# Optimization experiments

Measured on AMD Instinct MI355X. Metric: run time of the kernel, lower is better.

Reference implementation:

```python
import jax, jax.numpy as jnp
import numpy as np

NUM_HEADS = 16
EPS = 1e-5


def _ln(x, w, b):
    mu = jnp.mean(x, axis=-1, keepdims=True)
    var = jnp.mean((x - mu) ** 2, axis=-1, keepdims=True)
    return (x - mu) * jax.lax.rsqrt(var + EPS) * w + b


def _ada_ln(x, vol, lw, lb, gamma, beta, vs_w, vs_b):
    y = _ln(x, lw, lb)
    # volatility_scale: Linear(1,1) on vol[..., None] -> sigmoid
    vs = jax.nn.sigmoid(vol[..., None] * vs_w + vs_b)  # (B,S,1)
    return y * (1.0 + vs) * gamma + beta


def setup_inputs() -> dict:
    key = jax.random.key(0)
    ks = jax.random.split(key, 20)
    B, S, H = 8, 1024, 1024
    Hf = 4 * H
    Hg = H // 2
    w = lambda k, i, o: jax.random.normal(k, (i, o), jnp.float32) * 0.02
    inp = {
        'x': jax.random.normal(ks[0], (B, S, H), jnp.float32),
        'volatility': jax.random.uniform(ks[1], (B, S), jnp.float32),
        'Wq': w(ks[2], H, H), 'bq': jnp.zeros((H,), jnp.float32),
        'Wk': w(ks[3], H, H), 'bk': jnp.zeros((H,), jnp.float32),
        'Wv': w(ks[4], H, H), 'bv': jnp.zeros((H,), jnp.float32),
        'Wo': w(ks[5], H, H), 'bo': jnp.zeros((H,), jnp.float32),
        'ln1_w': jnp.ones((H,), jnp.float32), 'ln1_b': jnp.zeros((H,), jnp.float32),
        'gamma1': jnp.ones((), jnp.float32), 'beta1': jnp.zeros((), jnp.float32),
        'vs1_w': jnp.float32(0.3), 'vs1_b': jnp.float32(0.0),
        'ffn_w1': w(ks[6], H, Hf), 'ffn_b1': jnp.zeros((Hf,), jnp.float32),
        'ffn_w2': w(ks[7], Hf, H), 'ffn_b2': jnp.zeros((H,), jnp.float32),
        'gate_w1': w(ks[8], H, Hg), 'gate_b1': jnp.zeros((Hg,), jnp.float32),
        'gate_w2': w(ks[9], Hg, H), 'gate_b2': jnp.zeros((H,), jnp.float32),
        'ln2_w': jnp.ones((H,), jnp.float32), 'ln2_b': jnp.zeros((H,), jnp.float32),
        'gamma2': jnp.ones((), jnp.float32), 'beta2': jnp.zeros((), jnp.float32),
        'vs2_w': jnp.float32(0.3), 'vs2_b': jnp.float32(0.0),
    }
    return inp


def reference(x, volatility, Wq, bq, Wk, bk, Wv, bv, Wo, bo,
              ln1_w, ln1_b, gamma1, beta1, vs1_w, vs1_b,
              ffn_w1, ffn_b1, ffn_w2, ffn_b2,
              gate_w1, gate_b1, gate_w2, gate_b2,
              ln2_w, ln2_b, gamma2, beta2, vs2_w, vs2_b):
    B, S, H = x.shape
    nh = NUM_HEADS
    hd = H // nh
    scale = np.sqrt(hd).astype(np.float32)

    # self-attention (eval mode -> dropout is identity)
    Q = (x @ Wq + bq).reshape(B, S, nh, hd)
    K = (x @ Wk + bk).reshape(B, S, nh, hd)
    V = (x @ Wv + bv).reshape(B, S, nh, hd)
    scores = jnp.einsum('bqhd,bkhd->bhqk', Q, K) / scale
    attn = jax.nn.softmax(scores, axis=-1)
    ctx = jnp.einsum('bhqk,bkhd->bqhd', attn, V).reshape(B, S, H)
    attn_out = ctx @ Wo + bo

    x = x + attn_out
    x = _ada_ln(x, volatility, ln1_w, ln1_b, gamma1, beta1, vs1_w, vs1_b)

    # volatility-adaptive FFN (volatility present -> gated path)
    h = jax.nn.gelu(x @ ffn_w1 + ffn_b1, approximate=False)
    ffn_out = h @ ffn_w2 + ffn_b2
    g = jax.nn.sigmoid(jax.nn.relu(x @ gate_w1 + gate_b1) @ gate_w2 + gate_b2)
    ffn_res = ffn_out * g + x * (1.0 - g)

    x = x + ffn_res
    x = _ada_ln(x, volatility, ln2_w, ln2_b, gamma2, beta2, vs2_w, vs2_b)
    return x
```

## Files before the change

### kernel.cpp

```cpp
#include <hip/hip_runtime.h>
#include <hip/hip_bf16.h>
#include <math.h>


#define HDIM 1024
#define NHEAD 16
#define DHEAD 64
#define NBATCH 8
#define NSEQ 1024
#define NTOK (NBATCH * NSEQ)
#define QKVSTR 3072
#define LNEPS 1e-5f
#define LOG2E_8 0.180336880f

using f32x4 = __attribute__((ext_vector_type(4))) float;
using s16x8 = __attribute__((ext_vector_type(8))) short;
using u16x8 = __attribute__((ext_vector_type(8))) unsigned short;

enum { ACT_NONE = 0, ACT_GELU = 1, ACT_RELU = 2, ACT_SIG = 3 };

__device__ inline float bf2f(unsigned short u) {
    union { unsigned u; float f; } t; t.u = ((unsigned)u) << 16; return t.f;
}
__device__ inline unsigned short f2bf(float f) {
    __hip_bfloat16 h = __float2bfloat16(f);
    return *reinterpret_cast<unsigned short*>(&h);
}
__device__ inline float gelu_f(float t) {
    const float u = t * (0.7978845608f + 0.0356774081f * t * t);
    const float e = __expf(2.f * u);
    const float th = 1.f - 2.f / (e + 1.f);
    return 0.5f * t * (1.f + th);
}

#define GLDS16(g, l) __builtin_amdgcn_global_load_lds( \
    (__attribute__((address_space(1))) void*)(g),      \
    (__attribute__((address_space(3))) void*)(l), 16, 0, 0)
#define MFMA16(a, b, c) __builtin_amdgcn_mfma_f32_16x16x32_bf16(a, b, c, 0, 0, 0)
#define BAR() __builtin_amdgcn_s_barrier()
#define LGKM0() do { asm volatile("s_waitcnt lgkmcnt(0)" ::: "memory"); \
                     __builtin_amdgcn_sched_barrier(0); } while (0)

template<int N> __device__ __forceinline__ void vmwait() {
    asm volatile("s_waitcnt vmcnt(%0)" :: "i"(N) : "memory");
}

__global__ __launch_bounds__(256)
void cast_bf16_k(const float* __restrict__ in, unsigned short* __restrict__ out, int n4)
{
    for (int i = blockIdx.x * 256 + threadIdx.x; i < n4; i += gridDim.x * 256) {
        float4 v = ((const float4*)in)[i];
        ushort4 o;
        o.x = f2bf(v.x); o.y = f2bf(v.y); o.z = f2bf(v.z); o.w = f2bf(v.w);
        ((ushort4*)out)[i] = o;
    }
}

__global__ __launch_bounds__(256)
void concat3_k(const float* __restrict__ a, const float* __restrict__ b,
               const float* __restrict__ c, float* __restrict__ o)
{
    int i = blockIdx.x * 256 + threadIdx.x;
    o[i] = i < 1024 ? a[i] : (i < 2048 ? b[i - 1024] : c[i - 2048]);
}

__global__ __launch_bounds__(256)
void transpose_cast_k(const float* __restrict__ W, unsigned short* __restrict__ Wt,
                      int K, int N)
{
    __shared__ float tile[32][33];
    const int tx = threadIdx.x, ty = threadIdx.y;
    const int k0 = blockIdx.y * 32, n0 = blockIdx.x * 32;
#pragma unroll
    for (int r = 0; r < 32; r += 8)
        tile[ty + r][tx] = W[(size_t)(k0 + ty + r) * N + n0 + tx];
    __syncthreads();
#pragma unroll
    for (int r = 0; r < 32; r += 8)
        Wt[(size_t)(n0 + ty + r) * K + k0 + tx] = f2bf(tile[tx][ty + r]);
}

__global__ __launch_bounds__(256)
void transpose_cast4_k(const float* __restrict__ W0, const float* __restrict__ W1,
                       const float* __restrict__ W2, const float* __restrict__ W3,
                       unsigned short* __restrict__ Wt)
{
    __shared__ float tile[32][33];
    const int z = blockIdx.z;
    const float* W = z == 0 ? W0 : z == 1 ? W1 : z == 2 ? W2 : W3;
    unsigned short* dst = Wt + (size_t)z * HDIM * HDIM;
    const int tx = threadIdx.x, ty = threadIdx.y;
    const int k0 = blockIdx.y * 32, n0 = blockIdx.x * 32;
#pragma unroll
    for (int r = 0; r < 32; r += 8)
        tile[ty + r][tx] = W[(size_t)(k0 + ty + r) * HDIM + n0 + tx];
    __syncthreads();
#pragma unroll
    for (int r = 0; r < 32; r += 8)
        dst[(size_t)(n0 + ty + r) * HDIM + k0 + tx] = f2bf(tile[tx][ty + r]);
}

__global__ __launch_bounds__(256)
void transpose_v_k(const unsigned short* __restrict__ vb, unsigned short* __restrict__ vtb)
{
    __shared__ unsigned short t[64][72];
    const int tid = threadIdx.x;
    const int b = blockIdx.z, h = blockIdx.y;
    const int s0 = blockIdx.x * 64;
    {
        const int r = tid >> 3, c = (tid & 7) * 8;
        *(u16x8*)&t[r][c] =
            *(const u16x8*)&vb[((size_t)(b * NSEQ + s0 + r)) * QKVSTR + h * DHEAD + c];
        *(u16x8*)&t[r + 32][c] =
            *(const u16x8*)&vb[((size_t)(b * NSEQ + s0 + r + 32)) * QKVSTR + h * DHEAD + c];
    }
    __syncthreads();
    {
        const int d = tid & 63, sc = (tid >> 6) * 16;
        u16x8 o0, o1;
#pragma unroll
        for (int i = 0; i < 8; ++i) o0[i] = t[sc + i][d];
#pragma unroll
        for (int i = 0; i < 8; ++i) o1[i] = t[sc + 8 + i][d];
        unsigned short* dst = &vtb[((size_t)((b * NHEAD + h) * DHEAD + d)) * NSEQ + s0 + sc];
        *(u16x8*)dst = o0;
        *(u16x8*)(dst + 8) = o1;
    }
}

template<int BM, int ACT, bool HAS_ADD, bool OUT_BF>
__global__ __launch_bounds__(256, 4)
void gemm_hi_k(const unsigned short* __restrict__ A, const unsigned short* __restrict__ Bt,
               const float* __restrict__ bias, const float* __restrict__ add,
               void* __restrict__ Cv, int M, int N, int K, int nbx)
{
    constexpr int NREP = (BM == 128) ? 4 : 2;
    constexpr int AR = BM / 64;
    constexpr int VM = AR + 2;
    __shared__ alignas(16) unsigned short As[2][BM * 32];
    __shared__ alignas(16) unsigned short Bs[2][128 * 32];

    const int tid = threadIdx.x;
    const int lane = tid & 63;
    const int w = tid >> 6;
    const int wr = (BM == 128) ? (w >> 1) : 0;
    const int wcb = (BM == 128) ? ((w & 1) * 64) : (w * 32);
    const int chunk = gridDim.x >> 3;
    const int wg = (blockIdx.x & 7) * chunk + (blockIdx.x >> 3);
    const int m0 = (wg / nbx) * BM;
    const int n0 = (wg % nbx) * 128;

    const int fr = lane & 15;
    const int fo = lane >> 4;
    const int fo_swz8 = (fo ^ ((fr >> 1) & 3)) * 8;

    const int srow = tid >> 2;
    const int sg8 = ((tid & 3) ^ ((tid >> 3) & 3)) * 8;

    f32x4 acc[4][NREP] = {};

    auto stage = [&](int t) {
        const int buf = t & 1;
        const unsigned short* as_ = A + (size_t)(m0 + srow) * K + t * 32 + sg8;
        const unsigned short* bs_ = Bt + (size_t)(n0 + srow) * K + t * 32 + sg8;
        GLDS16(as_, &As[buf][(w * 16) * 32]);
        if constexpr (BM == 128)
            GLDS16(as_ + (size_t)64 * K, &As[buf][(64 + w * 16) * 32]);
        GLDS16(bs_, &Bs[buf][(w * 16) * 32]);
        GLDS16(bs_ + (size_t)64 * K, &Bs[buf][(64 + w * 16) * 32]);
    };

    const int NT = K / 32;
    stage(0);

    for (int t = 0; t < NT; ++t) {
        if (t + 1 < NT) { stage(t + 1); vmwait<VM>(); }
        else            { vmwait<0>(); }
        BAR();

        const int buf = t & 1;
        s16x8 af[4], bf[NREP];
#pragma unroll
        for (int i = 0; i < 4; ++i)
            af[i] = *(const s16x8*)(&As[buf][(wr * 64 + i * 16 + fr) * 32 + fo_swz8]);
#pragma unroll
        for (int j = 0; j < NREP; ++j)
            bf[j] = *(const s16x8*)(&Bs[buf][(wcb + j * 16 + fr) * 32 + fo_swz8]);

        __builtin_amdgcn_s_setprio(1);
#pragma unroll
        for (int i = 0; i < 4; ++i)
#pragma unroll
            for (int j = 0; j < NREP; ++j)
                acc[i][j] = MFMA16(af[i], bf[j], acc[i][j]);
        __builtin_amdgcn_s_setprio(0);

        LGKM0();
        BAR();
    }

    float bv[NREP];
#pragma unroll
    for (int j = 0; j < NREP; ++j)
        bv[j] = bias[n0 + wcb + j * 16 + fr];
#pragma unroll
    for (int i = 0; i < 4; ++i) {
#pragma unroll
        for (int j = 0; j < NREP; ++j) {
            const int gn = n0 + wcb + j * 16 + fr;
#pragma unroll
            for (int r = 0; r < 4; ++r) {
                const int gm = m0 + wr * 64 + i * 16 + fo * 4 + r;
                float t = acc[i][j][r] + bv[j];
                if (HAS_ADD) t += add[(size_t)gm * N + gn];
                if (ACT == ACT_GELU)      t = gelu_f(t);
                else if (ACT == ACT_RELU) t = fmaxf(t, 0.f);
                else if (ACT == ACT_SIG)  t = 1.f / (1.f + __expf(-t));
                if (OUT_BF) ((unsigned short*)Cv)[(size_t)gm * N + gn] = f2bf(t);
                else        ((float*)Cv)[(size_t)gm * N + gn] = t;
            }
        }
    }
}

__global__ __launch_bounds__(512, 6)
void attn_k(const unsigned short* __restrict__ QKVb, const unsigned short* __restrict__ Vtb,
            unsigned short* __restrict__ Cb)
{
    __shared__ alignas(16) unsigned short Ks[2][64 * 64];
    __shared__ alignas(16) unsigned short Vs[2][64 * 64];
    __shared__ alignas(16) unsigned short Ps[8][16 * 72];

    const int tid = threadIdx.x;
    const int lane = tid & 63;
    const int wid = tid >> 6;
    const int L = blockIdx.x;
    const int xcd = L & 7, s = L >> 3;
    const int bh = xcd + ((s >> 3) << 3);
    const int qt = s & 7;
    const int b = bh >> 4, h = bh & 15;
    const int q0 = qt * 128 + wid * 16;

    const int kcol = lane & 15;
    const int kofs = (lane >> 4) * 8;
    const size_t qoff = ((size_t)(b * NSEQ + q0 + kcol)) * QKVSTR + h * DHEAD + kofs;
    const s16x8 qf0 = *(const s16x8*)(QKVb + qoff);
    const s16x8 qf1 = *(const s16x8*)(QKVb + qoff + 32);

    f32x4 accO[4] = {};
    float mrow[4] = {-1e30f, -1e30f, -1e30f, -1e30f};
    float lsum[4] = {0.f, 0.f, 0.f, 0.f};

    const int lr = lane >> 3;
    const int swz8 = (((lane & 7) ^ lr)) * 8;
    const size_t kbase  = ((size_t)(b * NSEQ)) * QKVSTR + HDIM + h * DHEAD;
    const size_t vtbase = ((size_t)(bh * DHEAD)) * NSEQ;

    unsigned short* const pw = &Ps[wid][0];
    const int prow = (lane >> 4) * 4;

    auto stage = [&](int kt, int buf) {
        const int rowb = wid * 8;
        GLDS16(QKVb + kbase + (size_t)(kt * 64 + rowb + lr) * QKVSTR + swz8,
               Ks[buf] + rowb * 64);
        GLDS16(Vtb + vtbase + (size_t)(rowb + lr) * NSEQ + kt * 64 + swz8,
               Vs[buf] + rowb * 64);
    };

    stage(0, 0);
    asm volatile("s_waitcnt vmcnt(0)" ::: "memory");
    __syncthreads();

    for (int kt = 0; kt < NSEQ / 64; ++kt) {
        const int cur = kt & 1;
        if (kt + 1 < NSEQ / 64) stage(kt + 1, cur ^ 1);

        f32x4 sa[4];
#pragma unroll
        for (int jt = 0; jt < 4; ++jt) {
            const int kr = jt * 16 + kcol;
            const unsigned swz = ((unsigned)(kr & 7)) << 4;
            const s16x8 kf0 = *(const s16x8*)((const char*)Ks[cur] + kr * 128 + ((kofs * 2) ^ swz));
            const s16x8 kf1 = *(const s16x8*)((const char*)Ks[cur] + kr * 128 + ((64 + kofs * 2) ^ swz));
            f32x4 t = {};
            t = MFMA16(qf0, kf0, t);
            t = MFMA16(qf1, kf1, t);
            sa[jt] = t * LOG2E_8;
        }

        float lmax[4];
#pragma unroll
        for (int r = 0; r < 4; ++r)
            lmax[r] = fmaxf(fmaxf(sa[0][r], sa[1][r]), fmaxf(sa[2][r], sa[3][r]));
        const float guard = fmaxf(fmaxf(lmax[0] - mrow[0], lmax[1] - mrow[1]),
                                  fmaxf(lmax[2] - mrow[2], lmax[3] - mrow[3]));
        if (!__all(guard <= 8.f)) {
#pragma unroll
            for (int r = 0; r < 4; ++r) {
                float m = lmax[r];
                m = fmaxf(m, __shfl_xor(m, 1));
                m = fmaxf(m, __shfl_xor(m, 2));
                m = fmaxf(m, __shfl_xor(m, 4));
                m = fmaxf(m, __shfl_xor(m, 8));
                const float mn = fmaxf(mrow[r], m);
                const float corr = exp2f(mrow[r] - mn);
                mrow[r] = mn;
                lsum[r] *= corr;
#pragma unroll
                for (int dt = 0; dt < 4; ++dt) accO[dt][r] *= corr;
            }
        }
#pragma unroll
        for (int r = 0; r < 4; ++r) {
#pragma unroll
            for (int jt = 0; jt < 4; ++jt) {
                const float p = exp2f(sa[jt][r] - mrow[r]);
                pw[(prow + r) * 72 + jt * 16 + kcol] = f2bf(p);
                lsum[r] += p;
            }
        }

#pragma unroll
        for (int kc = 0; kc < 2; ++kc) {
            const s16x8 pa = *(const s16x8*)(pw + kcol * 72 + kc * 32 + kofs);
#pragma unroll
            for (int dt = 0; dt < 4; ++dt) {
                const int dr = dt * 16 + kcol;
                const unsigned swz = ((unsigned)(dr & 7)) << 4;
                const s16x8 vf = *(const s16x8*)((const char*)Vs[cur] + dr * 128 +
                                                 ((kc * 64 + kofs * 2) ^ swz));
                accO[dt] = MFMA16(pa, vf, accO[dt]);
            }
        }

        if (kt + 1 < NSEQ / 64) asm volatile("s_waitcnt vmcnt(0)" ::: "memory");
        __builtin_amdgcn_s_barrier();
    }

#pragma unroll
    for (int r = 0; r < 4; ++r) {
        lsum[r] += __shfl_xor(lsum[r], 1);
        lsum[r] += __shfl_xor(lsum[r], 2);
        lsum[r] += __shfl_xor(lsum[r], 4);
        lsum[r] += __shfl_xor(lsum[r], 8);
    }

    const size_t obase = ((size_t)(b * NSEQ + q0 + prow)) * HDIM + h * DHEAD;
#pragma unroll
    for (int r = 0; r < 4; ++r) {
        const float rl = 1.f / lsum[r];
#pragma unroll
        for (int dt = 0; dt < 4; ++dt)
            Cb[obase + (size_t)r * HDIM + dt * 16 + kcol] = f2bf(accO[dt][r] * rl);
    }
}

template<int MODE, bool WRITE_BF>
__global__ __launch_bounds__(256)
void adaln_k(const float* __restrict__ a,
             const unsigned short* __restrict__ fo_bf,
             const unsigned short* __restrict__ g_bf,
             const float* __restrict__ vol,
             const float* __restrict__ lw, const float* __restrict__ lb,
             const float* __restrict__ gm, const float* __restrict__ bt,
             const float* __restrict__ vsw, const float* __restrict__ vsb,
             float* __restrict__ out, unsigned short* __restrict__ out_bf)
{
    const int tok = blockIdx.x;
    const int tid = threadIdx.x;
    const size_t base = (size_t)tok * HDIM + tid * 4;
    float v[4];
    {
        float4 va = *(const float4*)&a[base];
        if (MODE == 1) {
            ushort4 uf = *(const ushort4*)&fo_bf[base];
            ushort4 ug = *(const ushort4*)&g_bf[base];
            float f0 = bf2f(uf.x), f1 = bf2f(uf.y), f2 = bf2f(uf.z), f3 = bf2f(uf.w);
            float g0 = bf2f(ug.x), g1 = bf2f(ug.y), g2 = bf2f(ug.z), g3 = bf2f(ug.w);
            v[0] = va.x * (2.f - g0) + f0 * g0;
            v[1] = va.y * (2.f - g1) + f1 * g1;
            v[2] = va.z * (2.f - g2) + f2 * g2;
            v[3] = va.w * (2.f - g3) + f3 * g3;
        } else {
            v[0] = va.x; v[1] = va.y; v[2] = va.z; v[3] = va.w;
        }
    }
    float sum = v[0] + v[1] + v[2] + v[3];
    float sq  = v[0]*v[0] + v[1]*v[1] + v[2]*v[2] + v[3]*v[3];
#pragma unroll
    for (int off = 32; off > 0; off >>= 1) {
        sum += __shfl_down(sum, off);
        sq  += __shfl_down(sq, off);
    }
    __shared__ float ssum[4], ssq[4];
    const int wid = tid >> 6, lane = tid & 63;
    if (lane == 0) { ssum[wid] = sum; ssq[wid] = sq; }
    __syncthreads();
    const float tsum = ssum[0] + ssum[1] + ssum[2] + ssum[3];
    const float tsq  = ssq[0]  + ssq[1]  + ssq[2]  + ssq[3];
    const float mu   = tsum * (1.f / 1024.f);
    const float var  = tsq * (1.f / 1024.f) - mu * mu;
    const float rstd = rsqrtf(var + LNEPS);
    const float vsv  = 1.f / (1.f + __expf(-(vol[tok] * vsw[0] + vsb[0])));
    const float sca  = (1.f + vsv) * gm[0];
    const float off2 = bt[0];
    const float4 lwv = *(const float4*)&lw[tid * 4];
    const float4 lbv = *(const float4*)&lb[tid * 4];
    float r0 = ((v[0] - mu) * rstd * lwv.x + lbv.x) * sca + off2;
    float r1 = ((v[1] - mu) * rstd * lwv.y + lbv.y) * sca + off2;
    float r2 = ((v[2] - mu) * rstd * lwv.z + lbv.z) * sca + off2;
    float r3 = ((v[3] - mu) * rstd * lwv.w + lbv.w) * sca + off2;
    *(float4*)&out[base] = make_float4(r0, r1, r2, r3);
    if (WRITE_BF) {
        ushort4 ob;
        ob.x = f2bf(r0); ob.y = f2bf(r1); ob.z = f2bf(r2); ob.w = f2bf(r3);
        *(ushort4*)&out_bf[base] = ob;
    }
}

extern "C" void kernel_launch(void* const* d_in, const int* in_sizes, int n_in,
                              void* d_out, int out_size, void* d_ws, size_t ws_size,
                              hipStream_t stream)
{
    (void)in_sizes; (void)n_in; (void)out_size; (void)ws_size;
    const float* x    = (const float*)d_in[0];
    const float* vol  = (const float*)d_in[1];
    const float* Wq   = (const float*)d_in[2];  const float* bq  = (const float*)d_in[3];
    const float* Wk   = (const float*)d_in[4];  const float* bk  = (const float*)d_in[5];
    const float* Wv   = (const float*)d_in[6];  const float* bv  = (const float*)d_in[7];
    const float* Wo   = (const float*)d_in[8];  const float* bo  = (const float*)d_in[9];
    const float* ln1w = (const float*)d_in[10]; const float* ln1b = (const float*)d_in[11];
    const float* gm1  = (const float*)d_in[12]; const float* be1 = (const float*)d_in[13];
    const float* vs1w = (const float*)d_in[14]; const float* vs1b = (const float*)d_in[15];
    const float* fw1  = (const float*)d_in[16]; const float* fb1 = (const float*)d_in[17];
    const float* fw2  = (const float*)d_in[18]; const float* fb2 = (const float*)d_in[19];
    const float* gw1  = (const float*)d_in[20]; const float* gb1 = (const float*)d_in[21];
    const float* gw2  = (const float*)d_in[22]; const float* gb2 = (const float*)d_in[23];
    const float* ln2w = (const float*)d_in[24]; const float* ln2b = (const float*)d_in[25];
    const float* gm2  = (const float*)d_in[26]; const float* be2 = (const float*)d_in[27];
    const float* vs2w = (const float*)d_in[28]; const float* vs2b = (const float*)d_in[29];

    char* w = (char*)d_ws;
    auto MB = [](size_t v) { return v << 20; };
    unsigned short* wtqkv = (unsigned short*)(w + MB(0));
    unsigned short* wto   = (unsigned short*)(w + MB(6));
    unsigned short* wtf1  = (unsigned short*)(w + MB(8));
    unsigned short* wtf2  = (unsigned short*)(w + MB(16));
    unsigned short* wtg1  = (unsigned short*)(w + MB(24));
    unsigned short* wtg2  = (unsigned short*)(w + MB(25));
    unsigned short* xb   = (unsigned short*)(w + MB(26));
    unsigned short* qkvb = (unsigned short*)(w + MB(42));
    unsigned short* vtb  = (unsigned short*)(w + MB(90));
    unsigned short* cxb  = (unsigned short*)(w + MB(106));
    float*          ao   = (float*)(w + MB(122));
    float*          x1   = (float*)(w + MB(42));
    unsigned short* x1b  = (unsigned short*)(w + MB(74));
    unsigned short* hb   = (unsigned short*)(w + MB(90));
    unsigned short* ffnb = (unsigned short*)(w + MB(154));
    unsigned short* ghb  = (unsigned short*)(w + MB(170));
    unsigned short* ggb  = (unsigned short*)(w + MB(26));
    float*          bqkv = (float*)(w + MB(184));

    dim3 blk(256);
    dim3 tb(32, 8);
    transpose_cast4_k<<<dim3(32, 32, 4), tb, 0, stream>>>(Wq, Wk, Wv, Wo, wtqkv);
    transpose_cast_k<<<dim3(4096/32, 1024/32), tb, 0, stream>>>(fw1, wtf1, 1024, 4096);
    transpose_cast_k<<<dim3(1024/32, 4096/32), tb, 0, stream>>>(fw2, wtf2, 4096, 1024);
    transpose_cast_k<<<dim3(512/32, 1024/32),  tb, 0, stream>>>(gw1, wtg1, 1024, 512);
    transpose_cast_k<<<dim3(1024/32, 512/32),  tb, 0, stream>>>(gw2, wtg2, 512, 1024);
    cast_bf16_k<<<2048, blk, 0, stream>>>(x, xb, NTOK * HDIM / 4);
    concat3_k<<<12, blk, 0, stream>>>(bq, bk, bv, bqkv);

    gemm_hi_k<128, ACT_NONE, false, true><<<dim3(24 * 64), blk, 0, stream>>>(
        xb, wtqkv, bqkv, nullptr, qkvb, NTOK, QKVSTR, HDIM, 24);
    transpose_v_k<<<dim3(NSEQ / 64, NHEAD, NBATCH), blk, 0, stream>>>(qkvb + 2048, vtb);
    attn_k<<<dim3(1024), 512, 0, stream>>>(qkvb, vtb, cxb);
    gemm_hi_k<64, ACT_NONE, true, false><<<dim3(128 * 8), blk, 0, stream>>>(
        cxb, wto, bo, x, ao, NTOK, HDIM, HDIM, 8);
    adaln_k<0, true><<<dim3(NTOK), blk, 0, stream>>>(
        ao, nullptr, nullptr, vol, ln1w, ln1b, gm1, be1, vs1w, vs1b, x1, x1b);
    gemm_hi_k<128, ACT_GELU, false, true><<<dim3(32 * 64), blk, 0, stream>>>(
        x1b, wtf1, fb1, nullptr, hb, NTOK, 4096, HDIM, 32);
    gemm_hi_k<64, ACT_NONE, false, true><<<dim3(128 * 8), blk, 0, stream>>>(
        hb, wtf2, fb2, nullptr, ffnb, NTOK, HDIM, 4096, 8);
    gemm_hi_k<64, ACT_RELU, false, true><<<dim3(128 * 4), blk, 0, stream>>>(
        x1b, wtg1, gb1, nullptr, ghb, NTOK, 512, HDIM, 4);
    gemm_hi_k<64, ACT_SIG, false, true><<<dim3(128 * 8), blk, 0, stream>>>(
        ghb, wtg2, gb2, nullptr, ggb, NTOK, HDIM, 512, 8);
    adaln_k<1, false><<<dim3(NTOK), blk, 0, stream>>>(
        x1, ffnb, ggb, vol, ln2w, ln2b, gm2, be2, vs2w, vs2b, (float*)d_out, nullptr);
}
```

Before: 463.9 us.

## Fuse FFN up-projection and gate first layer into one GEMM

Concatenates the transposed FFN W1 and gate W1 weights, and their biases, so that a single 128-row-tile GEMM produces both the GELU hidden and the ReLU gate hidden, using a per-column activation selector. A new lda parameter lets the downstream FFN2 and gate2 GEMMs read their halves from the shared 4608-wide buffer. This removes one kernel launch and a second pass over x1b, and replaces the small, poorly occupied gate GEMM with extra tiles in a large grid. It also drops the explicit LDS-count wait before the loop-end barrier and relies on compiler-inserted waits instead.

After: 473.0 us. About the same (+1.9%).

```diff
diff --git a/kernel.cpp b/kernel.cpp
--- a/kernel.cpp
+++ b/kernel.cpp
@@ -17,7 +17,7 @@
 using s16x8 = __attribute__((ext_vector_type(8))) short;
 using u16x8 = __attribute__((ext_vector_type(8))) unsigned short;
 
-enum { ACT_NONE = 0, ACT_GELU = 1, ACT_RELU = 2, ACT_SIG = 3 };
+enum { ACT_NONE = 0, ACT_GELU = 1, ACT_RELU = 2, ACT_SIG = 3, ACT_GR = 4 };
 
 __device__ inline float bf2f(unsigned short u) {
     union { unsigned u; float f; } t; t.u = ((unsigned)u) << 16; return t.f;
@@ -38,8 +38,6 @@
     (__attribute__((address_space(3))) void*)(l), 16, 0, 0)
 #define MFMA16(a, b, c) __builtin_amdgcn_mfma_f32_16x16x32_bf16(a, b, c, 0, 0, 0)
 #define BAR() __builtin_amdgcn_s_barrier()
-#define LGKM0() do { asm volatile("s_waitcnt lgkmcnt(0)" ::: "memory"); \
-                     __builtin_amdgcn_sched_barrier(0); } while (0)
 
 template<int N> __device__ __forceinline__ void vmwait() {
     asm volatile("s_waitcnt vmcnt(%0)" :: "i"(N) : "memory");
@@ -62,6 +60,14 @@
 {
     int i = blockIdx.x * 256 + threadIdx.x;
     o[i] = i < 1024 ? a[i] : (i < 2048 ? b[i - 1024] : c[i - 2048]);
+}
+
+__global__ __launch_bounds__(256)
+void concat2_k(const float* __restrict__ a, const float* __restrict__ b,
+               float* __restrict__ o)
+{
+    int i = blockIdx.x * 256 + threadIdx.x;
+    o[i] = i < 4096 ? a[i] : b[i - 4096];
 }
 
 __global__ __launch_bounds__(256)
@@ -132,7 +138,7 @@
 __global__ __launch_bounds__(256, 4)
 void gemm_hi_k(const unsigned short* __restrict__ A, const unsigned short* __restrict__ Bt,
                const float* __restrict__ bias, const float* __restrict__ add,
-               void* __restrict__ Cv, int M, int N, int K, int nbx)
+               void* __restrict__ Cv, int M, int N, int K, int lda, int nbx)
 {
     constexpr int NREP = (BM == 128) ? 4 : 2;
     constexpr int AR = BM / 64;
@@ -161,11 +167,11 @@
 
     auto stage = [&](int t) {
         const int buf = t & 1;
-        const unsigned short* as_ = A + (size_t)(m0 + srow) * K + t * 32 + sg8;
+        const unsigned short* as_ = A + (size_t)(m0 + srow) * lda + t * 32 + sg8;
         const unsigned short* bs_ = Bt + (size_t)(n0 + srow) * K + t * 32 + sg8;
         GLDS16(as_, &As[buf][(w * 16) * 32]);
         if constexpr (BM == 128)
-            GLDS16(as_ + (size_t)64 * K, &As[buf][(64 + w * 16) * 32]);
+            GLDS16(as_ + (size_t)64 * lda, &As[buf][(64 + w * 16) * 32]);
         GLDS16(bs_, &Bs[buf][(w * 16) * 32]);
         GLDS16(bs_ + (size_t)64 * K, &Bs[buf][(64 + w * 16) * 32]);
     };
@@ -195,7 +201,6 @@
                 acc[i][j] = MFMA16(af[i], bf[j], acc[i][j]);
         __builtin_amdgcn_s_setprio(0);
 
-        LGKM0();
         BAR();
     }
 
@@ -216,6 +221,7 @@
                 if (ACT == ACT_GELU)      t = gelu_f(t);
                 else if (ACT == ACT_RELU) t = fmaxf(t, 0.f);
                 else if (ACT == ACT_SIG)  t = 1.f / (1.f + __expf(-t));
+                else if (ACT == ACT_GR)   t = (gn < 4096) ? gelu_f(t) : fmaxf(t, 0.f);
                 if (OUT_BF) ((unsigned short*)Cv)[(size_t)gm * N + gn] = f2bf(t);
                 else        ((float*)Cv)[(size_t)gm * N + gn] = t;
             }
@@ -444,9 +450,9 @@
     auto MB = [](size_t v) { return v << 20; };
     unsigned short* wtqkv = (unsigned short*)(w + MB(0));
     unsigned short* wto   = (unsigned short*)(w + MB(6));
-    unsigned short* wtf1  = (unsigned short*)(w + MB(8));
-    unsigned short* wtf2  = (unsigned short*)(w + MB(16));
-    unsigned short* wtg1  = (unsigned short*)(w + MB(24));
+    unsigned short* wtfg  = (unsigned short*)(w + MB(8));
+    unsigned short* wtg1  = (unsigned short*)(w + MB(16));
+    unsigned short* wtf2  = (unsigned short*)(w + MB(17));
     unsigned short* wtg2  = (unsigned short*)(w + MB(25));
     unsigned short* xb   = (unsigned short*)(w + MB(26));
     unsigned short* qkvb = (unsigned short*)(w + MB(42));
@@ -455,38 +461,37 @@
     float*          ao   = (float*)(w + MB(122));
     float*          x1   = (float*)(w + MB(42));
     unsigned short* x1b  = (unsigned short*)(w + MB(74));
-    unsigned short* hb   = (unsigned short*)(w + MB(90));
-    unsigned short* ffnb = (unsigned short*)(w + MB(154));
-    unsigned short* ghb  = (unsigned short*)(w + MB(170));
+    unsigned short* hgb  = (unsigned short*)(w + MB(90));
+    unsigned short* ffnb = (unsigned short*)(w + MB(162));
     unsigned short* ggb  = (unsigned short*)(w + MB(26));
     float*          bqkv = (float*)(w + MB(184));
+    float*          bfg  = (float*)(w + MB(185));
 
     dim3 blk(256);
     dim3 tb(32, 8);
     transpose_cast4_k<<<dim3(32, 32, 4), tb, 0, stream>>>(Wq, Wk, Wv, Wo, wtqkv);
-    transpose_cast_k<<<dim3(4096/32, 1024/32), tb, 0, stream>>>(fw1, wtf1, 1024, 4096);
+    transpose_cast_k<<<dim3(4096/32, 1024/32), tb, 0, stream>>>(fw1, wtfg, 1024, 4096);
+    transpose_cast_k<<<dim3(512/32, 1024/32),  tb, 0, stream>>>(gw1, wtg1, 1024, 512);
     transpose_cast_k<<<dim3(1024/32, 4096/32), tb, 0, stream>>>(fw2, wtf2, 4096, 1024);
-    transpose_cast_k<<<dim3(512/32, 1024/32),  tb, 0, stream>>>(gw1, wtg1, 1024, 512);
     transpose_cast_k<<<dim3(1024/32, 512/32),  tb, 0, stream>>>(gw2, wtg2, 512, 1024);
     cast_bf16_k<<<2048, blk, 0, stream>>>(x, xb, NTOK * HDIM / 4);
     concat3_k<<<12, blk, 0, stream>>>(bq, bk, bv, bqkv);
+    concat2_k<<<18, blk, 0, stream>>>(fb1, gb1, bfg);
 
     gemm_hi_k<128, ACT_NONE, false, true><<<dim3(24 * 64), blk, 0, stream>>>(
-        xb, wtqkv, bqkv, nullptr, qkvb, NTOK, QKVSTR, HDIM, 24);
+        xb, wtqkv, bqkv, nullptr, qkvb, NTOK, QKVSTR, HDIM, HDIM, 24);
     transpose_v_k<<<dim3(NSEQ / 64, NHEAD, NBATCH), blk, 0, stream>>>(qkvb + 2048, vtb);
     attn_k<<<dim3(1024), 512, 0, stream>>>(qkvb, vtb, cxb);
     gemm_hi_k<64, ACT_NONE, true, false><<<dim3(128 * 8), blk, 0, stream>>>(
-        cxb, wto, bo, x, ao, NTOK, HDIM, HDIM, 8);
+        cxb, wto, bo, x, ao, NTOK, HDIM, HDIM, HDIM, 8);
     adaln_k<0, true><<<dim3(NTOK), blk, 0, stream>>>(
         ao, nullptr, nullptr, vol, ln1w, ln1b, gm1, be1, vs1w, vs1b, x1, x1b);
-    gemm_hi_k<128, ACT_GELU, false, true><<<dim3(32 * 64), blk, 0, stream>>>(
-        x1b, wtf1, fb1, nullptr, hb, NTOK, 4096, HDIM, 32);
+    gemm_hi_k<128, ACT_GR, false, true><<<dim3(36 * 64), blk, 0, stream>>>(
+        x1b, wtfg, bfg, nullptr, hgb, NTOK, 4608, HDIM, HDIM, 36);
     gemm_hi_k<64, ACT_NONE, false, true><<<dim3(128 * 8), blk, 0, stream>>>(
-        hb, wtf2, fb2, nullptr, ffnb, NTOK, HDIM, 4096, 8);
-    gemm_hi_k<64, ACT_RELU, false, true><<<dim3(128 * 4), blk, 0, stream>>>(
-        x1b, wtg1, gb1, nullptr, ghb, NTOK, 512, HDIM, 4);
+        hgb, wtf2, fb2, nullptr, ffnb, NTOK, HDIM, 4096, 4608, 8);
     gemm_hi_k<64, ACT_SIG, false, true><<<dim3(128 * 8), blk, 0, stream>>>(
-        ghb, wtg2, gb2, nullptr, ggb, NTOK, HDIM, 512, 8);
+        hgb + 4096, wtg2, gb2, nullptr, ggb, NTOK, HDIM, 512, 4608, 8);
     adaln_k<1, false><<<dim3(NTOK), blk, 0, stream>>>(
         x1, ffnb, ggb, vol, ln2w, ln2b, gm2, be2, vs2w, vs2b, (float*)d_out, nullptr);
 }
```
